# Kernel optimization log

Measured on AMD Instinct MI355X. Metric: run time of the kernel, lower is better.

Reference implementation:

```python
import jax, jax.numpy as jnp
import numpy as np

B, S, D, H = 2, 2048, 1024, 16
DK = D // H

def setup_inputs() -> dict:
    key = jax.random.key(0)
    ks = jax.random.split(key, 9)
    def lin(k, fan_in):
        bound = 1.0 / np.sqrt(fan_in)
        kw, kb = jax.random.split(k)
        w = jax.random.uniform(kw, (D, D), jnp.float32, -bound, bound)
        b = jax.random.uniform(kb, (D,), jnp.float32, -bound, bound)
        return w, b
    Wq_w, Wq_b = lin(ks[0], D)
    Wk_w, Wk_b = lin(ks[1], D)
    Wv_w, Wv_b = lin(ks[2], D)
    Wo_w, Wo_b = lin(ks[3], D)
    x = jax.random.normal(ks[4], (B, S, D), jnp.float32)
    mask = jnp.ones((B, 1, 1, S), jnp.int32)
    return {"x": x, "mask": mask,
            "Wq_w": Wq_w, "Wq_b": Wq_b, "Wk_w": Wk_w, "Wk_b": Wk_b,
            "Wv_w": Wv_w, "Wv_b": Wv_b, "Wo_w": Wo_w, "Wo_b": Wo_b}

def reference(x, mask, Wq_w, Wq_b, Wk_w, Wk_b, Wv_w, Wv_b, Wo_w, Wo_b):
    b, s, d = x.shape
    def split_heads(t):  # [B,S,D] -> [B,H,S,DK]
        return t.reshape(b, s, H, DK).transpose(0, 2, 1, 3)
    Q = split_heads(x @ Wq_w.T + Wq_b)
    K = split_heads(x @ Wk_w.T + Wk_b)
    V = split_heads(x @ Wv_w.T + Wv_b)
    scale = 1.0 / jnp.sqrt(jnp.float32(DK))
    scores = jnp.einsum('bhqd,bhkd->bhqk', Q, K) * scale  # [B,H,S,S]
    scores = jnp.where(mask == 0, jnp.float32(-1e9), scores)
    attn = jax.nn.softmax(scores, axis=-1)
    context = jnp.einsum('bhqk,bhkd->bhqd', attn, V)  # [B,H,S,DK]
    context = context.transpose(0, 2, 1, 3).reshape(b, s, d)
    return context @ Wo_w.T + Wo_b
```

## Files before the change

kernel.cpp:

```cpp
#include <hip/hip_runtime.h>
#include <hip/hip_bf16.h>


#define DEV __device__ __forceinline__

typedef __bf16 bf16_t;
typedef __bf16 bf16x4 __attribute__((ext_vector_type(4)));
typedef __bf16 bf16x8 __attribute__((ext_vector_type(8)));
typedef float f32x4 __attribute__((ext_vector_type(4)));
typedef float f32x16 __attribute__((ext_vector_type(16)));
typedef unsigned int u32;

constexpr int Ss = 2048, Dd = 1024, Hh = 16, DKk = 64;

DEV void gload_lds16(const void* g, void* l) {
  __builtin_amdgcn_global_load_lds(
      (__attribute__((address_space(1))) void*)(g),
      (__attribute__((address_space(3))) void*)(l), 16, 0, 0);
}

DEV bf16_t f2b(float v) { return (bf16_t)v; }

DEV u32 cvtpk(float lo, float hi) {
  u32 r;
  asm("v_cvt_pk_bf16_f32 %0, %1, %2" : "=v"(r) : "v"(lo), "v"(hi));
  return r;
}

DEV void swap32(u32& a, u32& b) {
  asm("v_permlane32_swap_b32 %0, %1" : "+v"(a), "+v"(b));
}

DEV float exp2_fast(float x) {
  float r;
  asm("v_exp_f32 %0, %1" : "=v"(r) : "v"(x));
  return r;
}

DEV void cvt16_core(const float* src, bf16_t* dst) {
  const float4* s4 = (const float4*)src;
  float4 a = s4[0], b = s4[1], c = s4[2], d = s4[3];
  bf16x8 lo = {f2b(a.x), f2b(a.y), f2b(a.z), f2b(a.w), f2b(b.x), f2b(b.y), f2b(b.z), f2b(b.w)};
  bf16x8 hi = {f2b(c.x), f2b(c.y), f2b(c.z), f2b(c.w), f2b(d.x), f2b(d.y), f2b(d.z), f2b(d.w)};
  *(bf16x8*)dst = lo;
  *(bf16x8*)(dst + 8) = hi;
}

__global__ __launch_bounds__(256) void cvt16(const float* __restrict__ x,
                                             bf16_t* __restrict__ xb) {
  size_t i = ((size_t)blockIdx.x * 256 + threadIdx.x) * 16;
  cvt16_core(x + i, xb + i);
}

__global__ __launch_bounds__(256) void cvt_all(
    const float* __restrict__ x,
    const float* __restrict__ wq, const float* __restrict__ wk,
    const float* __restrict__ wv, const float* __restrict__ wo,
    bf16_t* __restrict__ xb, bf16_t* __restrict__ Wb) {
  size_t i = ((size_t)blockIdx.x * 256 + threadIdx.x) * 16;
  const size_t XN = (size_t)4 << 20;
  if (i < XN) {
    cvt16_core(x + i, xb + i);
  } else {
    size_t j = i - XN;
    int z = (int)(j >> 20);
    size_t o = j & (((size_t)1 << 20) - 1);
    const float* s = (z == 0) ? wq : ((z == 1) ? wk : ((z == 2) ? wv : wo));
    cvt16_core(s + o, Wb + j);
  }
}

template <bool WB16>
__global__ __launch_bounds__(256) void gemm_qkv(
    const bf16_t* __restrict__ A,
    const float* __restrict__ W0, const float* __restrict__ W1, const float* __restrict__ W2,
    const bf16_t* __restrict__ Wb,
    const float* __restrict__ b0, const float* __restrict__ b1, const float* __restrict__ b2,
    bf16_t* __restrict__ o0, bf16_t* __restrict__ o1, bf16_t* __restrict__ o2) {
  const int fid = (int)((blockIdx.z * gridDim.y + blockIdx.y) * gridDim.x + blockIdx.x);
  const int swz = (fid & 7) * 96 + (fid >> 3);
  const int bx = swz & 7, by = (swz >> 3) & 31, z = swz >> 8;

  const float* Wf = (z == 0) ? W0 : ((z == 1) ? W1 : W2);
  const bf16_t* Wbf = Wb + (size_t)z * (1u << 20);
  const float* bias = (z == 0) ? b0 : ((z == 1) ? b1 : b2);
  bf16_t* out = (z == 0) ? o0 : ((z == 1) ? o1 : o2);
  const float scl = (z == 0) ? 0.18033688f : 1.0f;

  __shared__ __align__(16) bf16_t As[128 * 32];
  __shared__ __align__(16) bf16_t Ws[128 * 32];

  const int tid = threadIdx.x;
  const int lane = tid & 63, w = tid >> 6;
  const int quad = lane >> 4, c = lane & 15;
  const int wm = w >> 1, wn = w & 1;
  const int m0 = by * 128, n0 = bx * 128;
  const int trow = tid >> 1, tcol = (tid & 1) * 16;
  const int srow = lane >> 2, scol = (lane & 3) * 8;

  const f32x4 vzero = {0.f, 0.f, 0.f, 0.f};
  f32x4 acc[4][4];
  for (int i = 0; i < 4; i++)
    for (int j = 0; j < 4; j++) acc[i][j] = vzero;

  for (int k0 = 0; k0 < 1024; k0 += 32) {
    for (int r = 0; r < 2; r++) {
      int row = r * 64 + w * 16;
      gload_lds16(&A[(size_t)(m0 + row + srow) * 1024 + k0 + scol], &As[row * 32]);
      if (WB16)
        gload_lds16(&Wbf[(size_t)(n0 + row + srow) * 1024 + k0 + scol], &Ws[row * 32]);
    }
    if (!WB16)
      cvt16_core(&Wf[(size_t)(n0 + trow) * 1024 + k0 + tcol], &Ws[trow * 32 + tcol]);
    __syncthreads();

    bf16x8 af[4], bfr[4];
    for (int i = 0; i < 4; i++)
      af[i] = *(const bf16x8*)&As[(wm * 64 + i * 16 + c) * 32 + quad * 8];
    for (int j = 0; j < 4; j++)
      bfr[j] = *(const bf16x8*)&Ws[(wn * 64 + j * 16 + c) * 32 + quad * 8];
    for (int i = 0; i < 4; i++)
      for (int j = 0; j < 4; j++)
        acc[i][j] = __builtin_amdgcn_mfma_f32_16x16x32_bf16(af[i], bfr[j], acc[i][j], 0, 0, 0);
    __syncthreads();
  }

  for (int j = 0; j < 4; j++) {
    int n = n0 + wn * 64 + j * 16 + c;
    float bv = bias[n];
    for (int i = 0; i < 4; i++) {
      int mbase = m0 + wm * 64 + i * 16 + quad * 4;
      int b_ = mbase >> 11, s_ = mbase & 2047;
      int h_ = n >> 6, dk_ = n & 63;
      if (z < 2) {
        for (int r = 0; r < 4; r++)
          out[((size_t)(b_ * Hh + h_) * Ss + (s_ + r)) * DKk + dk_] =
              f2b((acc[i][j][r] + bv) * scl);
      } else {
        bf16x4 pk;
        for (int r = 0; r < 4; r++) pk[r] = f2b(acc[i][j][r] + bv);
        *(bf16x4*)&out[((size_t)(b_ * Hh + h_) * DKk + dk_) * Ss + s_] = pk;
      }
    }
  }
}

__global__ __launch_bounds__(512) void attn_fwd(
    const bf16_t* __restrict__ Q, const bf16_t* __restrict__ K,
    const bf16_t* __restrict__ Vt, const int* __restrict__ mask,
    bf16_t* __restrict__ ctx) {
  __shared__ __align__(16) bf16_t smem[2][2][2][64 * 64];

  const int tid = threadIdx.x, lane = tid & 63, w = tid >> 6;
  const int g = w >> 2, wl = w & 3;
  const int m = lane & 31, hi = lane >> 5;

  const int fid = (int)(blockIdx.y * gridDim.x + blockIdx.x);
  const int xcd = fid & 7, j_ = fid >> 3;
  const int bh = xcd * 4 + (j_ >> 4);
  const int qblk = j_ & 15;

  const int b_ = bh >> 4, h_ = bh & 15;
  const int q0 = qblk * 128 + wl * 32;
  const size_t head = (size_t)bh * Ss * DKk;
  const int* maskb = mask + b_ * Ss + g * 1024;
  const int kbase = g * 16;

  bf16_t (*Ksg)[64 * 64] = smem[0][g];
  bf16_t (*Vtg)[64 * 64] = smem[1][g];

  const int sr = lane >> 3;
  const int gc = (lane & 7) ^ sr;

  for (int r = 0; r < 2; r++) {
    int row = r * 32 + wl * 8;
    gload_lds16(&K[head + (size_t)(kbase * 64 + row + sr) * 64 + gc * 8], &Ksg[0][row * 64]);
    gload_lds16(&Vt[head + (size_t)(row + sr) * Ss + kbase * 64 + gc * 8], &Vtg[0][row * 64]);
  }

  bf16x8 qf[4];
#pragma unroll
  for (int ks = 0; ks < 4; ks++)
    qf[ks] = *(const bf16x8*)&Q[head + (size_t)(q0 + m) * 64 + ks * 16 + hi * 8];

  const bf16_t oneb = f2b(1.0f);
  const bf16x8 ones = {oneb, oneb, oneb, oneb, oneb, oneb, oneb, oneb};

  f32x16 o0, o1, ol;
#pragma unroll
  for (int i = 0; i < 16; i++) { o0[i] = 0.f; o1[i] = 0.f; ol[i] = 0.f; }

  constexpr int NTg = 16;
  for (int it = 0; it < NTg; it++) {
    const int cur = it & 1;
    __syncthreads();

    int mv = maskb[it * 64 + lane];

    if (it + 1 < NTg) {
      int nxt = cur ^ 1;
      int t = kbase + it + 1;
      for (int r = 0; r < 2; r++) {
        int row = r * 32 + wl * 8;
        gload_lds16(&K[head + (size_t)(t * 64 + row + sr) * 64 + gc * 8],
                    &Ksg[nxt][row * 64]);
        gload_lds16(&Vt[head + (size_t)(row + sr) * Ss + t * 64 + gc * 8],
                    &Vtg[nxt][row * 64]);
      }
    }

    f32x16 sc[2];
#pragma unroll
    for (int i = 0; i < 16; i++) { sc[0][i] = 0.f; sc[1][i] = 0.f; }

    __builtin_amdgcn_s_setprio(1);
#pragma unroll
    for (int ks = 0; ks < 4; ks++) {
      const int pc = ((ks * 2 + hi) ^ (m & 7)) * 8;
      bf16x8 k0 = *(const bf16x8*)&Ksg[cur][m * 64 + pc];
      bf16x8 k1 = *(const bf16x8*)&Ksg[cur][(32 + m) * 64 + pc];
      sc[0] = __builtin_amdgcn_mfma_f32_32x32x16_bf16(k0, qf[ks], sc[0], 0, 0, 0);
      sc[1] = __builtin_amdgcn_mfma_f32_32x32x16_bf16(k1, qf[ks], sc[1], 0, 0, 0);
    }
    __builtin_amdgcn_s_setprio(0);

    unsigned long long bits = __ballot(mv != 0);
    if (bits == ~0ull) {
#pragma unroll
      for (int nt = 0; nt < 2; nt++)
#pragma unroll
        for (int i = 0; i < 16; i++) sc[nt][i] = exp2_fast(sc[nt][i]);
    } else {
#pragma unroll
      for (int nt = 0; nt < 2; nt++) {
        u32 wb = (u32)(bits >> (nt * 32));
        u32 wsh = hi ? (wb >> 4) : wb;
#pragma unroll
        for (int i = 0; i < 16; i++) {
          int bitpos = 8 * (i >> 2) + (i & 3);
          sc[nt][i] = ((wsh >> bitpos) & 1u) ? exp2_fast(sc[nt][i]) : 0.f;
        }
      }
    }

    __builtin_amdgcn_s_setprio(1);
#pragma unroll
    for (int t = 0; t < 4; t++) {
      const int nt = t >> 1, gA = 2 * (t & 1), gB = gA + 1;
      u32 a0 = cvtpk(sc[nt][4 * gA + 0], sc[nt][4 * gA + 1]);
      u32 a1 = cvtpk(sc[nt][4 * gA + 2], sc[nt][4 * gA + 3]);
      u32 b0 = cvtpk(sc[nt][4 * gB + 0], sc[nt][4 * gB + 1]);
      u32 b1 = cvtpk(sc[nt][4 * gB + 2], sc[nt][4 * gB + 3]);
      swap32(a0, b0);
      swap32(a1, b1);
      int4 wv = {(int)a0, (int)a1, (int)b0, (int)b1};
      bf16x8 pa = __builtin_bit_cast(bf16x8, wv);

      ol = __builtin_amdgcn_mfma_f32_32x32x16_bf16(pa, ones, ol, 0, 0, 0);
      const int pc = ((t * 2 + hi) ^ (m & 7)) * 8;
      bf16x8 v0 = *(const bf16x8*)&Vtg[cur][m * 64 + pc];
      bf16x8 v1 = *(const bf16x8*)&Vtg[cur][(32 + m) * 64 + pc];
      o0 = __builtin_amdgcn_mfma_f32_32x32x16_bf16(pa, v0, o0, 0, 0, 0);
      o1 = __builtin_amdgcn_mfma_f32_32x32x16_bf16(pa, v1, o1, 0, 0, 0);
    }
    __builtin_amdgcn_s_setprio(0);
  }

  __syncthreads();
  f32x4* cmb = (f32x4*)smem;
  if (g == 1) {
#pragma unroll
    for (int c = 0; c < 4; c++) {
      f32x4 t0 = {o0[4 * c], o0[4 * c + 1], o0[4 * c + 2], o0[4 * c + 3]};
      f32x4 t1 = {o1[4 * c], o1[4 * c + 1], o1[4 * c + 2], o1[4 * c + 3]};
      f32x4 t2 = {ol[4 * c], ol[4 * c + 1], ol[4 * c + 2], ol[4 * c + 3]};
      cmb[(c + 0) * 256 + wl * 64 + lane] = t0;
      cmb[(c + 4) * 256 + wl * 64 + lane] = t1;
      cmb[(c + 8) * 256 + wl * 64 + lane] = t2;
    }
  }
  __syncthreads();
  if (g == 0) {
#pragma unroll
    for (int c = 0; c < 4; c++) {
      f32x4 p0 = cmb[(c + 0) * 256 + wl * 64 + lane];
      f32x4 p1 = cmb[(c + 4) * 256 + wl * 64 + lane];
      f32x4 p2 = cmb[(c + 8) * 256 + wl * 64 + lane];
#pragma unroll
      for (int k = 0; k < 4; k++) {
        o0[4 * c + k] += p0[k];
        o1[4 * c + k] += p1[k];
        ol[4 * c + k] += p2[k];
      }
    }
    f32x16 inv;
#pragma unroll
    for (int r = 0; r < 16; r++) inv[r] = 1.0f / ol[r];
#pragma unroll
    for (int r = 0; r < 16; r++) {
      int s_ = q0 + (r & 3) + 8 * (r >> 2) + 4 * hi;
      size_t base = ((size_t)(b_ * Ss + s_)) * Dd + h_ * 64;
      ctx[base + m] = f2b(o0[r] * inv[r]);
      ctx[base + 32 + m] = f2b(o1[r] * inv[r]);
    }
  }
}

template <bool WB16>
__global__ __launch_bounds__(256) void gemm_out(
    const bf16_t* __restrict__ A, const float* __restrict__ Wf,
    const bf16_t* __restrict__ Wb, const float* __restrict__ bias,
    float* __restrict__ out) {
  __shared__ __align__(16) bf16_t As[64 * 32];
  __shared__ __align__(16) bf16_t Ws[128 * 32];

  const int fid = (int)(blockIdx.y * gridDim.x + blockIdx.x);
  const int swz = (fid & 7) * 64 + (fid >> 3);
  const int bx = swz & 7, by = swz >> 3;

  const int tid = threadIdx.x;
  const int lane = tid & 63, w = tid >> 6;
  const int quad = lane >> 4, c = lane & 15;
  const int wm = w >> 1, wn = w & 1;
  const int m0 = by * 64, n0 = bx * 128;
  const int trow = tid >> 1, tcol = (tid & 1) * 16;
  const int srow = lane >> 2, scol = (lane & 3) * 8;

  const f32x4 vzero = {0.f, 0.f, 0.f, 0.f};
  f32x4 acc[2][4];
  for (int i = 0; i < 2; i++)
    for (int j = 0; j < 4; j++) acc[i][j] = vzero;

  for (int k0 = 0; k0 < 1024; k0 += 32) {
    gload_lds16(&A[(size_t)(m0 + w * 16 + srow) * 1024 + k0 + scol], &As[(w * 16) * 32]);
    if (WB16) {
      for (int r = 0; r < 2; r++) {
        int row = r * 64 + w * 16;
        gload_lds16(&Wb[(size_t)(n0 + row + srow) * 1024 + k0 + scol], &Ws[row * 32]);
      }
    } else {
      cvt16_core(&Wf[(size_t)(n0 + trow) * 1024 + k0 + tcol], &Ws[trow * 32 + tcol]);
    }
    __syncthreads();

    bf16x8 af[2], bfr[4];
    for (int i = 0; i < 2; i++)
      af[i] = *(const bf16x8*)&As[(wm * 32 + i * 16 + c) * 32 + quad * 8];
    for (int j = 0; j < 4; j++)
      bfr[j] = *(const bf16x8*)&Ws[(wn * 64 + j * 16 + c) * 32 + quad * 8];
    for (int i = 0; i < 2; i++)
      for (int j = 0; j < 4; j++)
        acc[i][j] = __builtin_amdgcn_mfma_f32_16x16x32_bf16(af[i], bfr[j], acc[i][j], 0, 0, 0);
    __syncthreads();
  }

  for (int j = 0; j < 4; j++) {
    int n = n0 + wn * 64 + j * 16 + c;
    float bv = bias[n];
    for (int i = 0; i < 2; i++) {
      int mbase = m0 + wm * 32 + i * 16 + quad * 4;
      for (int r = 0; r < 4; r++)
        out[(size_t)(mbase + r) * 1024 + n] = acc[i][j][r] + bv;
    }
  }
}

extern "C" void kernel_launch(void* const* d_in, const int* in_sizes, int n_in,
                              void* d_out, int out_size, void* d_ws, size_t ws_size,
                              hipStream_t stream) {
  const float* x  = (const float*)d_in[0];
  const int* mask = (const int*)d_in[1];
  const float* Wq = (const float*)d_in[2];
  const float* bq = (const float*)d_in[3];
  const float* Wk = (const float*)d_in[4];
  const float* bk = (const float*)d_in[5];
  const float* Wv = (const float*)d_in[6];
  const float* bv = (const float*)d_in[7];
  const float* Wo = (const float*)d_in[8];
  const float* bo = (const float*)d_in[9];
  float* out = (float*)d_out;

  bf16_t* ws = (bf16_t*)d_ws;
  const size_t QKV_ELEMS = (size_t)2 * Hh * Ss * DKk;
  bf16_t* xb  = ws;
  bf16_t* Qb  = ws + QKV_ELEMS;
  bf16_t* Kb  = ws + 2 * QKV_ELEMS;
  bf16_t* Vt  = ws + 3 * QKV_ELEMS;
  bf16_t* Wb  = ws + 4 * QKV_ELEMS;
  bf16_t* ctx = xb;

  const bool wb16 = ws_size >= (size_t)40 * 1024 * 1024;

  if (wb16) {
    cvt_all<<<dim3(2048), 256, 0, stream>>>(x, Wq, Wk, Wv, Wo, xb, Wb);
    gemm_qkv<true><<<dim3(8, 32, 3), 256, 0, stream>>>(
        xb, Wq, Wk, Wv, Wb, bq, bk, bv, Qb, Kb, Vt);
  } else {
    cvt16<<<dim3(1024), 256, 0, stream>>>(x, xb);
    gemm_qkv<false><<<dim3(8, 32, 3), 256, 0, stream>>>(
        xb, Wq, Wk, Wv, ws , bq, bk, bv, Qb, Kb, Vt);
  }
  attn_fwd<<<dim3(Ss / 128, 2 * Hh), 512, 0, stream>>>(Qb, Kb, Vt, mask, ctx);
  if (wb16)
    gemm_out<true><<<dim3(8, 64), 256, 0, stream>>>(ctx, Wo, Wb + 3 * (1u << 20), bo, out);
  else
    gemm_out<false><<<dim3(8, 64), 256, 0, stream>>>(ctx, Wo, ws , bo, out);
}
```

Before: 187.1 us.

## Triple-buffer K/V tiles with vmcnt waits and specialize unmasked path

Replaces the double-buffered K/Vt LDS pipeline with a three-stage ring that prefetches two tiles ahead. A raw s_barrier is preceded by explicit vmcnt waits, so the loads for later tiles stay in flight instead of being drained by __syncthreads. The mask is prechecked once per block and a templated path with no ballot or mask loads runs when every entry is set. LDS use grows to 96KB, which may lower occupancy, and the hand-counted vmcnt values are fragile.

```diff
diff --git a/kernel.cpp b/kernel.cpp
--- a/kernel.cpp
+++ b/kernel.cpp
@@ -145,69 +145,45 @@
   }
 }
 
-__global__ __launch_bounds__(512) void attn_fwd(
-    const bf16_t* __restrict__ Q, const bf16_t* __restrict__ K,
-    const bf16_t* __restrict__ Vt, const int* __restrict__ mask,
-    bf16_t* __restrict__ ctx) {
-  __shared__ __align__(16) bf16_t smem[2][2][2][64 * 64];
-
-  const int tid = threadIdx.x, lane = tid & 63, w = tid >> 6;
-  const int g = w >> 2, wl = w & 3;
-  const int m = lane & 31, hi = lane >> 5;
-
-  const int fid = (int)(blockIdx.y * gridDim.x + blockIdx.x);
-  const int xcd = fid & 7, j_ = fid >> 3;
-  const int bh = xcd * 4 + (j_ >> 4);
-  const int qblk = j_ & 15;
-
-  const int b_ = bh >> 4, h_ = bh & 15;
-  const int q0 = qblk * 128 + wl * 32;
-  const size_t head = (size_t)bh * Ss * DKk;
-  const int* maskb = mask + b_ * Ss + g * 1024;
-  const int kbase = g * 16;
-
-  bf16_t (*Ksg)[64 * 64] = smem[0][g];
-  bf16_t (*Vtg)[64 * 64] = smem[1][g];
-
-  const int sr = lane >> 3;
-  const int gc = (lane & 7) ^ sr;
-
-  for (int r = 0; r < 2; r++) {
-    int row = r * 32 + wl * 8;
-    gload_lds16(&K[head + (size_t)(kbase * 64 + row + sr) * 64 + gc * 8], &Ksg[0][row * 64]);
-    gload_lds16(&Vt[head + (size_t)(row + sr) * Ss + kbase * 64 + gc * 8], &Vtg[0][row * 64]);
-  }
-
-  bf16x8 qf[4];
-#pragma unroll
-  for (int ks = 0; ks < 4; ks++)
-    qf[ks] = *(const bf16x8*)&Q[head + (size_t)(q0 + m) * 64 + ks * 16 + hi * 8];
-
-  const bf16_t oneb = f2b(1.0f);
-  const bf16x8 ones = {oneb, oneb, oneb, oneb, oneb, oneb, oneb, oneb};
-
-  f32x16 o0, o1, ol;
-#pragma unroll
-  for (int i = 0; i < 16; i++) { o0[i] = 0.f; o1[i] = 0.f; ol[i] = 0.f; }
-
-  constexpr int NTg = 16;
-  for (int it = 0; it < NTg; it++) {
-    const int cur = it & 1;
-    __syncthreads();
-
-    int mv = maskb[it * 64 + lane];
-
-    if (it + 1 < NTg) {
-      int nxt = cur ^ 1;
-      int t = kbase + it + 1;
-      for (int r = 0; r < 2; r++) {
-        int row = r * 32 + wl * 8;
-        gload_lds16(&K[head + (size_t)(t * 64 + row + sr) * 64 + gc * 8],
-                    &Ksg[nxt][row * 64]);
-        gload_lds16(&Vt[head + (size_t)(row + sr) * Ss + t * 64 + gc * 8],
-                    &Vtg[nxt][row * 64]);
-      }
-    }
+template <bool MASKED>
+DEV void attn_main(const bf16_t* __restrict__ Kp, const bf16_t* __restrict__ Vtp,
+                   const int* __restrict__ maskb, size_t head, int kbase,
+                   bf16_t (*Ksg)[64 * 64], bf16_t (*Vtg)[64 * 64],
+                   const bf16x8 (&qf)[4], bf16x8 ones,
+                   f32x16& o0, f32x16& o1, f32x16& ol,
+                   int lane, int wl, int sr, int gc, int m, int hi) {
+  auto stage = [&](int t, int b) {
+    int tt = kbase + t;
+    for (int r = 0; r < 2; r++) {
+      int row = r * 32 + wl * 8;
+      gload_lds16(&Kp[head + (size_t)(tt * 64 + row + sr) * 64 + gc * 8],
+                  &Ksg[b][row * 64]);
+      gload_lds16(&Vtp[head + (size_t)(row + sr) * Ss + tt * 64 + gc * 8],
+                  &Vtg[b][row * 64]);
+    }
+  };
+
+  int mvq[3] = {1, 1, 1};
+  stage(0, 0);
+  if (MASKED) mvq[0] = maskb[0 * 64 + lane];
+  stage(1, 1);
+  if (MASKED) mvq[1] = maskb[1 * 64 + lane];
+
+#pragma unroll
+  for (int it = 0; it < 16; ++it) {
+    const int b = it % 3;
+    if (it < 15) {
+      if (MASKED) asm volatile("s_waitcnt vmcnt(5)" ::: "memory");
+      else        asm volatile("s_waitcnt vmcnt(4)" ::: "memory");
+    } else {
+      asm volatile("s_waitcnt vmcnt(0)" ::: "memory");
+    }
+    __builtin_amdgcn_s_barrier();
+    if (it + 2 < 16) {
+      stage(it + 2, (it + 2) % 3);
+      if (MASKED) mvq[(it + 2) % 3] = maskb[(it + 2) * 64 + lane];
+    }
+    __builtin_amdgcn_sched_barrier(0);
 
     f32x16 sc[2];
 #pragma unroll
@@ -217,28 +193,35 @@
 #pragma unroll
     for (int ks = 0; ks < 4; ks++) {
       const int pc = ((ks * 2 + hi) ^ (m & 7)) * 8;
-      bf16x8 k0 = *(const bf16x8*)&Ksg[cur][m * 64 + pc];
-      bf16x8 k1 = *(const bf16x8*)&Ksg[cur][(32 + m) * 64 + pc];
+      bf16x8 k0 = *(const bf16x8*)&Ksg[b][m * 64 + pc];
+      bf16x8 k1 = *(const bf16x8*)&Ksg[b][(32 + m) * 64 + pc];
       sc[0] = __builtin_amdgcn_mfma_f32_32x32x16_bf16(k0, qf[ks], sc[0], 0, 0, 0);
       sc[1] = __builtin_amdgcn_mfma_f32_32x32x16_bf16(k1, qf[ks], sc[1], 0, 0, 0);
     }
     __builtin_amdgcn_s_setprio(0);
 
-    unsigned long long bits = __ballot(mv != 0);
-    if (bits == ~0ull) {
+    if (!MASKED) {
 #pragma unroll
       for (int nt = 0; nt < 2; nt++)
 #pragma unroll
         for (int i = 0; i < 16; i++) sc[nt][i] = exp2_fast(sc[nt][i]);
     } else {
-#pragma unroll
-      for (int nt = 0; nt < 2; nt++) {
-        u32 wb = (u32)(bits >> (nt * 32));
-        u32 wsh = hi ? (wb >> 4) : wb;
-#pragma unroll
-        for (int i = 0; i < 16; i++) {
-          int bitpos = 8 * (i >> 2) + (i & 3);
-          sc[nt][i] = ((wsh >> bitpos) & 1u) ? exp2_fast(sc[nt][i]) : 0.f;
+      unsigned long long bits = __ballot(mvq[b] != 0);
+      if (bits == ~0ull) {
+#pragma unroll
+        for (int nt = 0; nt < 2; nt++)
+#pragma unroll
+          for (int i = 0; i < 16; i++) sc[nt][i] = exp2_fast(sc[nt][i]);
+      } else {
+#pragma unroll
+        for (int nt = 0; nt < 2; nt++) {
+          u32 wb = (u32)(bits >> (nt * 32));
+          u32 wsh = hi ? (wb >> 4) : wb;
+#pragma unroll
+          for (int i = 0; i < 16; i++) {
+            int bitpos = 8 * (i >> 2) + (i & 3);
+            sc[nt][i] = ((wsh >> bitpos) & 1u) ? exp2_fast(sc[nt][i]) : 0.f;
+          }
         }
       }
     }
@@ -258,16 +241,70 @@
 
       ol = __builtin_amdgcn_mfma_f32_32x32x16_bf16(pa, ones, ol, 0, 0, 0);
       const int pc = ((t * 2 + hi) ^ (m & 7)) * 8;
-      bf16x8 v0 = *(const bf16x8*)&Vtg[cur][m * 64 + pc];
-      bf16x8 v1 = *(const bf16x8*)&Vtg[cur][(32 + m) * 64 + pc];
+      bf16x8 v0 = *(const bf16x8*)&Vtg[b][m * 64 + pc];
+      bf16x8 v1 = *(const bf16x8*)&Vtg[b][(32 + m) * 64 + pc];
       o0 = __builtin_amdgcn_mfma_f32_32x32x16_bf16(pa, v0, o0, 0, 0, 0);
       o1 = __builtin_amdgcn_mfma_f32_32x32x16_bf16(pa, v1, o1, 0, 0, 0);
     }
     __builtin_amdgcn_s_setprio(0);
   }
+}
+
+__global__ __launch_bounds__(512) void attn_fwd(
+    const bf16_t* __restrict__ Q, const bf16_t* __restrict__ K,
+    const bf16_t* __restrict__ Vt, const int* __restrict__ mask,
+    bf16_t* __restrict__ ctx) {
+  __shared__ __align__(16) bf16_t KsS[2][3][64 * 64];
+  __shared__ __align__(16) bf16_t VtS[2][3][64 * 64];
+
+  const int tid = threadIdx.x, lane = tid & 63, w = tid >> 6;
+  const int g = w >> 2, wl = w & 3;
+  const int m = lane & 31, hi = lane >> 5;
+
+  const int fid = (int)(blockIdx.y * gridDim.x + blockIdx.x);
+  const int xcd = fid & 7, j_ = fid >> 3;
+  const int bh = xcd * 4 + (j_ >> 4);
+  const int qblk = j_ & 15;
+
+  const int b_ = bh >> 4, h_ = bh & 15;
+  const int q0 = qblk * 128 + wl * 32;
+  const size_t head = (size_t)bh * Ss * DKk;
+  const int* maskb = mask + b_ * Ss + g * 1024;
+  const int kbase = g * 16;
+
+  bf16_t (*Ksg)[64 * 64] = KsS[g];
+  bf16_t (*Vtg)[64 * 64] = VtS[g];
+
+  const int sr = lane >> 3;
+  const int gc = (lane & 7) ^ sr;
+
+  bf16x8 qf[4];
+#pragma unroll
+  for (int ks = 0; ks < 4; ks++)
+    qf[ks] = *(const bf16x8*)&Q[head + (size_t)(q0 + m) * 64 + ks * 16 + hi * 8];
+
+  const bf16_t oneb = f2b(1.0f);
+  const bf16x8 ones = {oneb, oneb, oneb, oneb, oneb, oneb, oneb, oneb};
+
+  f32x16 o0, o1, ol;
+#pragma unroll
+  for (int i = 0; i < 16; i++) { o0[i] = 0.f; o1[i] = 0.f; ol[i] = 0.f; }
+
+  bool allone = true;
+  for (int it = 0; it < 16; ++it) {
+    int v = maskb[it * 64 + lane];
+    allone &= (__ballot(v != 0) == ~0ull);
+  }
+
+  if (allone)
+    attn_main<false>(K, Vt, maskb, head, kbase, Ksg, Vtg, qf, ones,
+                     o0, o1, ol, lane, wl, sr, gc, m, hi);
+  else
+    attn_main<true>(K, Vt, maskb, head, kbase, Ksg, Vtg, qf, ones,
+                    o0, o1, ol, lane, wl, sr, gc, m, hi);
 
   __syncthreads();
-  f32x4* cmb = (f32x4*)smem;
+  f32x4* cmb = (f32x4*)KsS;
   if (g == 1) {
 #pragma unroll
     for (int c = 0; c < 4; c++) {
```

Measured after the change: 187.8 us. Within noise of the previous version (+0.4%).

## Shrink attention tiles to 64 queries and 32-key blocks with 256-thread blocks

Applied to the files above, without the earlier changes.

Restructures the attention kernel so each block handles 64 queries with two wave groups (4 waves) instead of 128 queries with 8 waves, and streams 32-key tiles instead of 64-key tiles, doubling the grid to 1024 blocks. The V tile staging and swizzle are reworked to fit the smaller 32x64 LDS buffers. This aims at more blocks in flight and lower LDS use per block, at the cost of loading K/V twice as often per query and more barriers per key.

```diff
diff --git a/kernel.cpp b/kernel.cpp
--- a/kernel.cpp
+++ b/kernel.cpp
@@ -145,38 +145,47 @@
   }
 }
 
-__global__ __launch_bounds__(512) void attn_fwd(
+__global__ __launch_bounds__(256) void attn_fwd(
     const bf16_t* __restrict__ Q, const bf16_t* __restrict__ K,
     const bf16_t* __restrict__ Vt, const int* __restrict__ mask,
     bf16_t* __restrict__ ctx) {
-  __shared__ __align__(16) bf16_t smem[2][2][2][64 * 64];
+  __shared__ __align__(16) bf16_t smem[2][2][2][32 * 64];
 
   const int tid = threadIdx.x, lane = tid & 63, w = tid >> 6;
-  const int g = w >> 2, wl = w & 3;
+  const int g = w >> 1, gw = w & 1;
   const int m = lane & 31, hi = lane >> 5;
 
   const int fid = (int)(blockIdx.y * gridDim.x + blockIdx.x);
   const int xcd = fid & 7, j_ = fid >> 3;
-  const int bh = xcd * 4 + (j_ >> 4);
-  const int qblk = j_ & 15;
+  const int bh = xcd * 4 + (j_ >> 5);
+  const int qblk = j_ & 31;
 
   const int b_ = bh >> 4, h_ = bh & 15;
-  const int q0 = qblk * 128 + wl * 32;
+  const int q0 = qblk * 64 + gw * 32;
   const size_t head = (size_t)bh * Ss * DKk;
   const int* maskb = mask + b_ * Ss + g * 1024;
-  const int kbase = g * 16;
-
-  bf16_t (*Ksg)[64 * 64] = smem[0][g];
-  bf16_t (*Vtg)[64 * 64] = smem[1][g];
-
-  const int sr = lane >> 3;
-  const int gc = (lane & 7) ^ sr;
-
-  for (int r = 0; r < 2; r++) {
-    int row = r * 32 + wl * 8;
-    gload_lds16(&K[head + (size_t)(kbase * 64 + row + sr) * 64 + gc * 8], &Ksg[0][row * 64]);
-    gload_lds16(&Vt[head + (size_t)(row + sr) * Ss + kbase * 64 + gc * 8], &Vtg[0][row * 64]);
-  }
+  const int kbase = g * 32;
+
+  bf16_t (*Ksg)[32 * 64] = smem[0][g];
+  bf16_t (*Vtg)[32 * 64] = smem[1][g];
+
+  const int sl_r = lane >> 3, sl_p = lane & 7;
+
+  auto stage = [&](int t, int bufi) {
+    const int kt = kbase + t;
+#pragma unroll
+    for (int i = 0; i < 2; i++) {
+      const int rb = gw * 16 + i * 8;
+      const int r = rb + sl_r;
+      const int gk = sl_p ^ (r & 7);
+      gload_lds16(&K[head + (size_t)(kt * 32 + r) * 64 + gk * 8],
+                  &Ksg[bufi][rb * 64]);
+      const int dk = r + 32 * (gk >> 2);
+      const int kc = gk & 3;
+      gload_lds16(&Vt[head + (size_t)dk * Ss + kt * 32 + kc * 8],
+                  &Vtg[bufi][rb * 64]);
+    }
+  };
 
   bf16x8 qf[4];
 #pragma unroll
@@ -190,76 +199,62 @@
 #pragma unroll
   for (int i = 0; i < 16; i++) { o0[i] = 0.f; o1[i] = 0.f; ol[i] = 0.f; }
 
-  constexpr int NTg = 16;
+  stage(0, 0);
+
+  constexpr int NTg = 32;
   for (int it = 0; it < NTg; it++) {
     const int cur = it & 1;
     __syncthreads();
 
-    int mv = maskb[it * 64 + lane];
-
-    if (it + 1 < NTg) {
-      int nxt = cur ^ 1;
-      int t = kbase + it + 1;
-      for (int r = 0; r < 2; r++) {
-        int row = r * 32 + wl * 8;
-        gload_lds16(&K[head + (size_t)(t * 64 + row + sr) * 64 + gc * 8],
-                    &Ksg[nxt][row * 64]);
-        gload_lds16(&Vt[head + (size_t)(row + sr) * Ss + t * 64 + gc * 8],
-                    &Vtg[nxt][row * 64]);
-      }
-    }
-
-    f32x16 sc[2];
-#pragma unroll
-    for (int i = 0; i < 16; i++) { sc[0][i] = 0.f; sc[1][i] = 0.f; }
+    if (it + 1 < NTg) stage(it + 1, cur ^ 1);
+
+    int mv = maskb[it * 32 + m];
+
+    f32x16 sc;
+#pragma unroll
+    for (int i = 0; i < 16; i++) sc[i] = 0.f;
 
     __builtin_amdgcn_s_setprio(1);
 #pragma unroll
     for (int ks = 0; ks < 4; ks++) {
       const int pc = ((ks * 2 + hi) ^ (m & 7)) * 8;
-      bf16x8 k0 = *(const bf16x8*)&Ksg[cur][m * 64 + pc];
-      bf16x8 k1 = *(const bf16x8*)&Ksg[cur][(32 + m) * 64 + pc];
-      sc[0] = __builtin_amdgcn_mfma_f32_32x32x16_bf16(k0, qf[ks], sc[0], 0, 0, 0);
-      sc[1] = __builtin_amdgcn_mfma_f32_32x32x16_bf16(k1, qf[ks], sc[1], 0, 0, 0);
+      bf16x8 kf = *(const bf16x8*)&Ksg[cur][m * 64 + pc];
+      sc = __builtin_amdgcn_mfma_f32_32x32x16_bf16(kf, qf[ks], sc, 0, 0, 0);
     }
     __builtin_amdgcn_s_setprio(0);
 
     unsigned long long bits = __ballot(mv != 0);
     if (bits == ~0ull) {
 #pragma unroll
-      for (int nt = 0; nt < 2; nt++)
-#pragma unroll
-        for (int i = 0; i < 16; i++) sc[nt][i] = exp2_fast(sc[nt][i]);
+      for (int i = 0; i < 16; i++) sc[i] = exp2_fast(sc[i]);
     } else {
-#pragma unroll
-      for (int nt = 0; nt < 2; nt++) {
-        u32 wb = (u32)(bits >> (nt * 32));
-        u32 wsh = hi ? (wb >> 4) : wb;
-#pragma unroll
-        for (int i = 0; i < 16; i++) {
-          int bitpos = 8 * (i >> 2) + (i & 3);
-          sc[nt][i] = ((wsh >> bitpos) & 1u) ? exp2_fast(sc[nt][i]) : 0.f;
-        }
+      u32 wb = (u32)bits;
+      u32 wsh = hi ? (wb >> 4) : wb;
+#pragma unroll
+      for (int i = 0; i < 16; i++) {
+        int bitpos = 8 * (i >> 2) + (i & 3);
+        sc[i] = ((wsh >> bitpos) & 1u) ? exp2_fast(sc[i]) : 0.f;
       }
     }
 
     __builtin_amdgcn_s_setprio(1);
 #pragma unroll
-    for (int t = 0; t < 4; t++) {
-      const int nt = t >> 1, gA = 2 * (t & 1), gB = gA + 1;
-      u32 a0 = cvtpk(sc[nt][4 * gA + 0], sc[nt][4 * gA + 1]);
-      u32 a1 = cvtpk(sc[nt][4 * gA + 2], sc[nt][4 * gA + 3]);
-      u32 b0 = cvtpk(sc[nt][4 * gB + 0], sc[nt][4 * gB + 1]);
-      u32 b1 = cvtpk(sc[nt][4 * gB + 2], sc[nt][4 * gB + 3]);
+    for (int t = 0; t < 2; t++) {
+      const int base = 8 * t;
+      u32 a0 = cvtpk(sc[base + 0], sc[base + 1]);
+      u32 a1 = cvtpk(sc[base + 2], sc[base + 3]);
+      u32 b0 = cvtpk(sc[base + 4], sc[base + 5]);
+      u32 b1 = cvtpk(sc[base + 6], sc[base + 7]);
       swap32(a0, b0);
       swap32(a1, b1);
       int4 wv = {(int)a0, (int)a1, (int)b0, (int)b1};
       bf16x8 pa = __builtin_bit_cast(bf16x8, wv);
 
       ol = __builtin_amdgcn_mfma_f32_32x32x16_bf16(pa, ones, ol, 0, 0, 0);
-      const int pc = ((t * 2 + hi) ^ (m & 7)) * 8;
-      bf16x8 v0 = *(const bf16x8*)&Vtg[cur][m * 64 + pc];
-      bf16x8 v1 = *(const bf16x8*)&Vtg[cur][(32 + m) * 64 + pc];
+      const int pc0 = ((t * 2 + hi) ^ (m & 7)) * 8;
+      const int pc1 = ((4 + t * 2 + hi) ^ (m & 7)) * 8;
+      bf16x8 v0 = *(const bf16x8*)&Vtg[cur][m * 64 + pc0];
+      bf16x8 v1 = *(const bf16x8*)&Vtg[cur][m * 64 + pc1];
       o0 = __builtin_amdgcn_mfma_f32_32x32x16_bf16(pa, v0, o0, 0, 0, 0);
       o1 = __builtin_amdgcn_mfma_f32_32x32x16_bf16(pa, v1, o1, 0, 0, 0);
     }
@@ -274,18 +269,18 @@
       f32x4 t0 = {o0[4 * c], o0[4 * c + 1], o0[4 * c + 2], o0[4 * c + 3]};
       f32x4 t1 = {o1[4 * c], o1[4 * c + 1], o1[4 * c + 2], o1[4 * c + 3]};
       f32x4 t2 = {ol[4 * c], ol[4 * c + 1], ol[4 * c + 2], ol[4 * c + 3]};
-      cmb[(c + 0) * 256 + wl * 64 + lane] = t0;
-      cmb[(c + 4) * 256 + wl * 64 + lane] = t1;
-      cmb[(c + 8) * 256 + wl * 64 + lane] = t2;
+      cmb[(c + 0) * 128 + gw * 64 + lane] = t0;
+      cmb[(c + 4) * 128 + gw * 64 + lane] = t1;
+      cmb[(c + 8) * 128 + gw * 64 + lane] = t2;
     }
   }
   __syncthreads();
   if (g == 0) {
 #pragma unroll
     for (int c = 0; c < 4; c++) {
-      f32x4 p0 = cmb[(c + 0) * 256 + wl * 64 + lane];
-      f32x4 p1 = cmb[(c + 4) * 256 + wl * 64 + lane];
-      f32x4 p2 = cmb[(c + 8) * 256 + wl * 64 + lane];
+      f32x4 p0 = cmb[(c + 0) * 128 + gw * 64 + lane];
+      f32x4 p1 = cmb[(c + 4) * 128 + gw * 64 + lane];
+      f32x4 p2 = cmb[(c + 8) * 128 + gw * 64 + lane];
 #pragma unroll
       for (int k = 0; k < 4; k++) {
         o0[4 * c + k] += p0[k];
@@ -400,7 +395,7 @@
     gemm_qkv<false><<<dim3(8, 32, 3), 256, 0, stream>>>(
         xb, Wq, Wk, Wv, ws , bq, bk, bv, Qb, Kb, Vt);
   }
-  attn_fwd<<<dim3(Ss / 128, 2 * Hh), 512, 0, stream>>>(Qb, Kb, Vt, mask, ctx);
+  attn_fwd<<<dim3(32, 32), 256, 0, stream>>>(Qb, Kb, Vt, mask, ctx);
   if (wb16)
     gemm_out<true><<<dim3(8, 64), 256, 0, stream>>>(ctx, Wo, Wb + 3 * (1u << 20), bo, out);
   else
```

After: 203.9 us. 1.09x slower.

## Load K and V tiles directly from global memory instead of staging in LDS

Applied to the files above, without the earlier changes.

Removes the double-buffered LDS staging of K and Vt tiles in the attention kernel. Each wave now reads its K and V fragments straight from global memory, relying on L1/L2 caching, and the per-iteration __syncthreads is dropped. Shared memory shrinks to just the cross-group combine buffer, which may raise occupancy. In exchange, each of the four waves per group re-reads the same K/V data from cache, and there is no explicit prefetch to hide global load latency.

```diff
diff --git a/kernel.cpp b/kernel.cpp
--- a/kernel.cpp
+++ b/kernel.cpp
@@ -149,7 +149,7 @@
     const bf16_t* __restrict__ Q, const bf16_t* __restrict__ K,
     const bf16_t* __restrict__ Vt, const int* __restrict__ mask,
     bf16_t* __restrict__ ctx) {
-  __shared__ __align__(16) bf16_t smem[2][2][2][64 * 64];
+  __shared__ __align__(16) f32x4 cmb[12 * 256];
 
   const int tid = threadIdx.x, lane = tid & 63, w = tid >> 6;
   const int g = w >> 2, wl = w & 3;
@@ -164,19 +164,11 @@
   const int q0 = qblk * 128 + wl * 32;
   const size_t head = (size_t)bh * Ss * DKk;
   const int* maskb = mask + b_ * Ss + g * 1024;
-  const int kbase = g * 16;
-
-  bf16_t (*Ksg)[64 * 64] = smem[0][g];
-  bf16_t (*Vtg)[64 * 64] = smem[1][g];
-
-  const int sr = lane >> 3;
-  const int gc = (lane & 7) ^ sr;
-
-  for (int r = 0; r < 2; r++) {
-    int row = r * 32 + wl * 8;
-    gload_lds16(&K[head + (size_t)(kbase * 64 + row + sr) * 64 + gc * 8], &Ksg[0][row * 64]);
-    gload_lds16(&Vt[head + (size_t)(row + sr) * Ss + kbase * 64 + gc * 8], &Vtg[0][row * 64]);
-  }
+
+  const bf16_t* kp0 = K + head + (size_t)(g * 1024 + m) * 64 + hi * 8;
+  const bf16_t* kp1 = kp0 + 32 * 64;
+  const bf16_t* vp0 = Vt + head + (size_t)m * Ss + g * 1024 + hi * 8;
+  const bf16_t* vp1 = vp0 + (size_t)32 * Ss;
 
   bf16x8 qf[4];
 #pragma unroll
@@ -192,23 +184,8 @@
 
   constexpr int NTg = 16;
   for (int it = 0; it < NTg; it++) {
-    const int cur = it & 1;
-    __syncthreads();
-
     int mv = maskb[it * 64 + lane];
 
-    if (it + 1 < NTg) {
-      int nxt = cur ^ 1;
-      int t = kbase + it + 1;
-      for (int r = 0; r < 2; r++) {
-        int row = r * 32 + wl * 8;
-        gload_lds16(&K[head + (size_t)(t * 64 + row + sr) * 64 + gc * 8],
-                    &Ksg[nxt][row * 64]);
-        gload_lds16(&Vt[head + (size_t)(row + sr) * Ss + t * 64 + gc * 8],
-                    &Vtg[nxt][row * 64]);
-      }
-    }
-
     f32x16 sc[2];
 #pragma unroll
     for (int i = 0; i < 16; i++) { sc[0][i] = 0.f; sc[1][i] = 0.f; }
@@ -216,9 +193,8 @@
     __builtin_amdgcn_s_setprio(1);
 #pragma unroll
     for (int ks = 0; ks < 4; ks++) {
-      const int pc = ((ks * 2 + hi) ^ (m & 7)) * 8;
-      bf16x8 k0 = *(const bf16x8*)&Ksg[cur][m * 64 + pc];
-      bf16x8 k1 = *(const bf16x8*)&Ksg[cur][(32 + m) * 64 + pc];
+      bf16x8 k0 = *(const bf16x8*)(kp0 + ks * 16);
+      bf16x8 k1 = *(const bf16x8*)(kp1 + ks * 16);
       sc[0] = __builtin_amdgcn_mfma_f32_32x32x16_bf16(k0, qf[ks], sc[0], 0, 0, 0);
       sc[1] = __builtin_amdgcn_mfma_f32_32x32x16_bf16(k1, qf[ks], sc[1], 0, 0, 0);
     }
@@ -256,18 +232,21 @@
       int4 wv = {(int)a0, (int)a1, (int)b0, (int)b1};
       bf16x8 pa = __builtin_bit_cast(bf16x8, wv);
 
+      bf16x8 v0 = *(const bf16x8*)(vp0 + t * 16);
+      bf16x8 v1 = *(const bf16x8*)(vp1 + t * 16);
       ol = __builtin_amdgcn_mfma_f32_32x32x16_bf16(pa, ones, ol, 0, 0, 0);
-      const int pc = ((t * 2 + hi) ^ (m & 7)) * 8;
-      bf16x8 v0 = *(const bf16x8*)&Vtg[cur][m * 64 + pc];
-      bf16x8 v1 = *(const bf16x8*)&Vtg[cur][(32 + m) * 64 + pc];
       o0 = __builtin_amdgcn_mfma_f32_32x32x16_bf16(pa, v0, o0, 0, 0, 0);
       o1 = __builtin_amdgcn_mfma_f32_32x32x16_bf16(pa, v1, o1, 0, 0, 0);
     }
     __builtin_amdgcn_s_setprio(0);
+
+    kp0 += 64 * 64;
+    kp1 += 64 * 64;
+    vp0 += 64;
+    vp1 += 64;
   }
 
   __syncthreads();
-  f32x4* cmb = (f32x4*)smem;
   if (g == 1) {
 #pragma unroll
     for (int c = 0; c < 4; c++) {
```

Result: slower. 264.4 us (+41.3%).
